# Performance work log

Measured on AMD Instinct MI355X. Metric: run time of the kernel, lower is better.

Reference implementation:

```python
import jax, jax.numpy as jnp
import numpy as np

N = 100000
E = 1600000
F_IN = 128
DIM = 32
NUM_CLASSES = 40
BN_EPS = 1e-5


def setup_inputs() -> dict:
    key = jax.random.key(0)
    ks = jax.random.split(key, 16)
    inp = {}
    inp['x'] = jax.random.normal(ks[0], (N, F_IN), dtype=jnp.float32)
    inp['edge_index'] = jax.random.randint(ks[1], (2, E), 0, N, dtype=jnp.int64)
    s = lambda fan_in: 1.0 / np.sqrt(fan_in)
    # GINConv 1 MLP: Linear(F_IN, DIM) -> ReLU -> Linear(DIM, DIM)
    inp['w1a'] = jax.random.uniform(ks[2], (F_IN, DIM), jnp.float32, -s(F_IN), s(F_IN))
    inp['b1a'] = jnp.zeros((DIM,), jnp.float32)
    inp['w1b'] = jax.random.uniform(ks[3], (DIM, DIM), jnp.float32, -s(DIM), s(DIM))
    inp['b1b'] = jnp.zeros((DIM,), jnp.float32)
    # GINConv 2 MLP: Linear(DIM, DIM) -> ReLU -> Linear(DIM, DIM)
    inp['w2a'] = jax.random.uniform(ks[4], (DIM, DIM), jnp.float32, -s(DIM), s(DIM))
    inp['b2a'] = jnp.zeros((DIM,), jnp.float32)
    inp['w2b'] = jax.random.uniform(ks[5], (DIM, DIM), jnp.float32, -s(DIM), s(DIM))
    inp['b2b'] = jnp.zeros((DIM,), jnp.float32)
    # BatchNorm params (eval mode: running stats)
    inp['bn1_g'] = jnp.ones((DIM,), jnp.float32)
    inp['bn1_b'] = jnp.zeros((DIM,), jnp.float32)
    inp['bn1_m'] = jax.random.normal(ks[6], (DIM,), jnp.float32) * 0.1
    inp['bn1_v'] = jax.random.uniform(ks[7], (DIM,), jnp.float32, 0.5, 1.5)
    inp['bn2_g'] = jnp.ones((DIM,), jnp.float32)
    inp['bn2_b'] = jnp.zeros((DIM,), jnp.float32)
    inp['bn2_m'] = jax.random.normal(ks[8], (DIM,), jnp.float32) * 0.1
    inp['bn2_v'] = jax.random.uniform(ks[9], (DIM,), jnp.float32, 0.5, 1.5)
    # FC heads
    inp['fc1_w'] = jax.random.uniform(ks[10], (DIM, DIM), jnp.float32, -s(DIM), s(DIM))
    inp['fc1_b'] = jnp.zeros((DIM,), jnp.float32)
    inp['fc2_w'] = jax.random.uniform(ks[11], (DIM, NUM_CLASSES), jnp.float32, -s(DIM), s(DIM))
    inp['fc2_b'] = jnp.zeros((NUM_CLASSES,), jnp.float32)
    return inp


def _gin_conv(x, src, dst, wa, ba, wb, bb):
    # sum-aggregate neighbor features (messages flow src -> dst), eps = 0
    agg = jax.ops.segment_sum(x[src], dst, num_segments=N)
    h = agg + x  # (1 + eps) * x + sum_j x_j
    h = jax.nn.relu(h @ wa + ba)
    return h @ wb + bb


def _bn(x, g, b, m, v):
    return (x - m) * (g * jax.lax.rsqrt(v + BN_EPS)) + b


def reference(x, edge_index, w1a, b1a, w1b, b1b, w2a, b2a, w2b, b2b,
              bn1_g, bn1_b, bn1_m, bn1_v, bn2_g, bn2_b, bn2_m, bn2_v,
              fc1_w, fc1_b, fc2_w, fc2_b):
    src, dst = edge_index[0], edge_index[1]
    h = jax.nn.relu(_gin_conv(x, src, dst, w1a, b1a, w1b, b1b))
    h = _bn(h, bn1_g, bn1_b, bn1_m, bn1_v)  # dropout is identity in eval
    h = _gin_conv(h, src, dst, w2a, b2a, w2b, b2b)
    h = _bn(h, bn2_g, bn2_b, bn2_m, bn2_v)
    h = jax.nn.relu(h @ fc1_w + fc1_b)
    logits = h @ fc2_w + fc2_b
    return jax.nn.log_softmax(logits, axis=1)
```

## Files before the change

kernel.cpp:

```cpp
#include <hip/hip_runtime.h>
#include <hip/hip_bf16.h>

static constexpr int N_   = 100000;
static constexpr int E_   = 1600000;
static constexpr int FIN_ = 128;
static constexpr int DIM_ = 32;
static constexpr int NC_  = 40;
static constexpr int NB_BKT = (N_ + 127) / 128;
static constexpr int NCHUNK = 256;
static constexpr int EPC    = E_ / NCHUNK;
static constexpr int NB64P  = 1564;
static constexpr int CS_NB  = (NB_BKT + 7) / 8;

__device__ __forceinline__ int edge_at(const void* e, int is64, long long i) {
    return is64 ? (int)((const long long*)e)[i] : ((const int*)e)[i];
}

__device__ __forceinline__ float bflo(unsigned u) { return __uint_as_float(u << 16); }
__device__ __forceinline__ float bfhi(unsigned u) { return __uint_as_float(u & 0xffff0000u); }

__device__ __forceinline__ unsigned pack2bf(float a, float b) {
    __hip_bfloat16 ha = __float2bfloat16(a), hb = __float2bfloat16(b);
    unsigned ua = *(const unsigned short*)&ha, ub = *(const unsigned short*)&hb;
    return ua | (ub << 16);
}

#define DETECT_FLAG(edge, sflag)                                        \
    if (threadIdx.x < 64) {                                             \
        const long long* p_ = (const long long*)(edge);                 \
        long long v_ = p_[threadIdx.x];                                 \
        bool bad_ = (v_ < 0 || v_ >= (long long)N_);                    \
        unsigned long long m_ = __ballot(bad_);                         \
        if (threadIdx.x == 0) sflag = (m_ == 0ull) ? 1 : 0;             \
    }                                                                   \
    __syncthreads();

__device__ __forceinline__ void stage_acc2(const float* __restrict__ Asm,
                                           const float* __restrict__ Wsm,
                                           int nq, int d0, float4 acc[2]) {
#pragma unroll
    for (int kc = 0; kc < 8; ++kc) {
        float4 w0 = *(const float4*)&Wsm[(kc * 4 + 0) * 32 + d0];
        float4 w1 = *(const float4*)&Wsm[(kc * 4 + 1) * 32 + d0];
        float4 w2 = *(const float4*)&Wsm[(kc * 4 + 2) * 32 + d0];
        float4 w3 = *(const float4*)&Wsm[(kc * 4 + 3) * 32 + d0];
#pragma unroll
        for (int i = 0; i < 2; ++i) {
            float4 a = *(const float4*)&Asm[(nq + 32 * i) * 36 + kc * 4];
            acc[i].x += a.x * w0.x + a.y * w1.x + a.z * w2.x + a.w * w3.x;
            acc[i].y += a.x * w0.y + a.y * w1.y + a.z * w2.y + a.w * w3.y;
            acc[i].z += a.x * w0.z + a.y * w1.z + a.z * w2.z + a.w * w3.z;
            acc[i].w += a.x * w0.w + a.y * w1.w + a.z * w2.w + a.w * w3.w;
        }
    }
}

__global__ __launch_bounds__(256) void chist_kernel(const void* __restrict__ edge,
                                                    int* __restrict__ ghist) {
    __shared__ int lh[NB_BKT];
    __shared__ int sflag;
    DETECT_FLAG(edge, sflag)
    for (int i = threadIdx.x; i < NB_BKT; i += 256) lh[i] = 0;
    __syncthreads();
    int f = sflag;
    int b = blockIdx.x;
    int end = b * EPC + EPC;
    for (int e = b * EPC + threadIdx.x; e < end; e += 256) {
        int d = edge_at(edge, f, (long long)E_ + e);
        atomicAdd(&lh[d >> 7], 1);
    }
    __syncthreads();
    for (int i = threadIdx.x; i < NB_BKT; i += 256) ghist[b * NB_BKT + i] = lh[i];
}

__global__ __launch_bounds__(256) void colscan_kernel(const int* __restrict__ ghist,
                                                      int* __restrict__ gcur,
                                                      int* __restrict__ bcnt,
                                                      int* __restrict__ bbase,
                                                      int* __restrict__ offs,
                                                      int* __restrict__ done) {
    __shared__ int tile[256 * 9];
    __shared__ int a[256];
    __shared__ int lastFlag;
    int tid = threadIdx.x;
    int k0 = blockIdx.x * 8;

    {
        int kk = tid & 7, r0 = tid >> 3;
        for (int p = 0; p < 8; ++p) {
            int b = r0 + p * 32;
            int k = k0 + kk;
            tile[b * 9 + kk] = (k < NB_BKT) ? ghist[b * NB_BKT + k] : 0;
        }
    }
    __syncthreads();

    int c = tid >> 5, lane = tid & 31;
    int v[8]; int s = 0;
#pragma unroll
    for (int r = 0; r < 8; ++r) { v[r] = tile[(lane * 8 + r) * 9 + c]; s += v[r]; }
    int incl = s;
#pragma unroll
    for (int off = 1; off < 32; off <<= 1) {
        int u = __shfl_up(incl, off, 32);
        if (lane >= off) incl += u;
    }
    int ex = incl - s;
    int k = k0 + c;
    if (k < NB_BKT) {
        int run = ex;
#pragma unroll
        for (int r = 0; r < 8; ++r) {
            int b = lane * 8 + r;
            gcur[b * NB_BKT + k] = run;
            run += v[r];
        }
        if (lane == 31) bcnt[k] = run;
    }
    __syncthreads();
    if (tid == 0) {
        __threadfence();
        int old = atomicAdd(done, 1);
        lastFlag = (old == CS_NB - 1) ? 1 : 0;
    }
    __syncthreads();
    if (lastFlag) {
        __threadfence();
        int b4[4]; int base4 = tid * 4; int t = 0;
#pragma unroll
        for (int j = 0; j < 4; ++j) { int i = base4 + j; b4[j] = (i < NB_BKT) ? bcnt[i] : 0; t += b4[j]; }
        a[tid] = t;
        __syncthreads();
        for (int off = 1; off < 256; off <<= 1) {
            int u = a[tid] + ((tid >= off) ? a[tid - off] : 0);
            __syncthreads(); a[tid] = u; __syncthreads();
        }
        int g = a[tid] - t;
#pragma unroll
        for (int j = 0; j < 4; ++j) { int i = base4 + j; if (i < NB_BKT) bbase[i] = g; g += b4[j]; }
        if (tid == 255) offs[N_] = a[255];
    }
}

__global__ __launch_bounds__(256) void dscatter_kernel(const void* __restrict__ edge,
                                                       const int* __restrict__ bbase,
                                                       const int* __restrict__ gcur,
                                                       int* __restrict__ packed) {
    __shared__ int cur[NB_BKT];
    __shared__ int sflag;
    DETECT_FLAG(edge, sflag)
    int b = blockIdx.x, tid = threadIdx.x;
    for (int k = tid; k < NB_BKT; k += 256) cur[k] = bbase[k] + gcur[b * NB_BKT + k];
    __syncthreads();
    int f = sflag;
    int end = b * EPC + EPC;
    for (int e = b * EPC + tid; e < end; e += 256) {
        int s = edge_at(edge, f, e);
        int d = edge_at(edge, f, (long long)E_ + e);
        int pos = atomicAdd(&cur[d >> 7], 1);
        packed[pos] = s | ((d & 127) << 17);
    }
}

__global__ __launch_bounds__(256) void bsort_kernel(const int* __restrict__ bcnt,
                                                    const int* __restrict__ bbase,
                                                    const int* __restrict__ packed,
                                                    int* __restrict__ offs,
                                                    int* __restrict__ csr) {
    __shared__ int c[128];
    __shared__ int cur[128];
    int tid = threadIdx.x;
    int b = blockIdx.x;
    int beg = bbase[b], cnt = bcnt[b];
    if (tid < 128) c[tid] = 0;
    __syncthreads();
    for (int i = tid; i < cnt; i += 256)
        atomicAdd(&c[packed[beg + i] >> 17], 1);
    __syncthreads();
    int myv = (tid < 128) ? c[tid] : 0;
    for (int off = 1; off < 128; off <<= 1) {
        int t = 0;
        if (tid < 128) t = c[tid] + ((tid >= off) ? c[tid - off] : 0);
        __syncthreads();
        if (tid < 128) c[tid] = t;
        __syncthreads();
    }
    if (tid < 128) {
        int ex = c[tid] - myv;
        cur[tid] = ex;
        int node = b * 128 + tid;
        if (node < N_) offs[node] = beg + ex;
    }
    __syncthreads();
    for (int i = tid; i < cnt; i += 256) {
        int v = packed[beg + i];
        int p = atomicAdd(&cur[v >> 17], 1);
        csr[beg + p] = v & 0x1FFFF;
    }
}

__global__ __launch_bounds__(256) void proj_kernel(const float* __restrict__ x,
                                                   const float* __restrict__ w,
                                                   __hip_bfloat16* __restrict__ yh) {
    __shared__ __align__(16) float wsm[FIN_ * DIM_];
    __shared__ __align__(16) float xs[64 * 36];
    int tid = threadIdx.x;
    {
        const float4* w4 = (const float4*)w;
        float4* ws4 = (float4*)wsm;
        for (int i = tid; i < FIN_ * DIM_ / 4; i += 256) ws4[i] = w4[i];
    }
    int nodeBase = blockIdx.x * 64;
    int nq = tid >> 3, dq = tid & 7, d0 = dq * 4;
    const float4* x4 = (const float4*)x;

    float4 acc[2];
    acc[0] = make_float4(0.f, 0.f, 0.f, 0.f);
    acc[1] = make_float4(0.f, 0.f, 0.f, 0.f);

    for (int ch = 0; ch < 4; ++ch) {
        __syncthreads();
#pragma unroll
        for (int p = 0; p < 2; ++p) {
            int idx = tid + 256 * p;
            int row = idx >> 3, c4 = idx & 7;
            int gn = nodeBase + row; if (gn >= N_) gn = N_ - 1;
            *(float4*)&xs[row * 36 + c4 * 4] = x4[(size_t)gn * 32 + ch * 8 + c4];
        }
        __syncthreads();
        stage_acc2(xs, wsm + ch * 32 * DIM_, nq, d0, acc);
    }
#pragma unroll
    for (int i = 0; i < 2; ++i) {
        int gn = nodeBase + nq + 32 * i;
        uint2 pk;
        pk.x = pack2bf(acc[i].x, acc[i].y);
        pk.y = pack2bf(acc[i].z, acc[i].w);
        *(uint2*)((char*)yh + (size_t)gn * 64 + d0 * 2) = pk;
    }
}

__device__ __forceinline__ void gather_row(const int* __restrict__ csr,
                                           const char* __restrict__ vb,
                                           int beg, int end, int loff,
                                           float& a0, float& a1, float& a2, float& a3) {
    int i = beg;
    for (; i + 3 < end; i += 4) {
        int s0 = csr[i], s1 = csr[i + 1], s2 = csr[i + 2], s3 = csr[i + 3];
        uint2 u0 = *(const uint2*)(vb + (((size_t)s0) << 6) + loff);
        uint2 u1 = *(const uint2*)(vb + (((size_t)s1) << 6) + loff);
        uint2 u2 = *(const uint2*)(vb + (((size_t)s2) << 6) + loff);
        uint2 u3 = *(const uint2*)(vb + (((size_t)s3) << 6) + loff);
        a0 += (bflo(u0.x) + bflo(u1.x)) + (bflo(u2.x) + bflo(u3.x));
        a1 += (bfhi(u0.x) + bfhi(u1.x)) + (bfhi(u2.x) + bfhi(u3.x));
        a2 += (bflo(u0.y) + bflo(u1.y)) + (bflo(u2.y) + bflo(u3.y));
        a3 += (bfhi(u0.y) + bfhi(u1.y)) + (bfhi(u2.y) + bfhi(u3.y));
    }
    for (; i < end; ++i) {
        int s0 = csr[i];
        uint2 u0 = *(const uint2*)(vb + (((size_t)s0) << 6) + loff);
        a0 += bflo(u0.x); a1 += bfhi(u0.x); a2 += bflo(u0.y); a3 += bfhi(u0.y);
    }
}

__global__ __launch_bounds__(256) void gathu_kernel(const int* __restrict__ offs,
                                                    const int* __restrict__ csr,
                                                    const __hip_bfloat16* __restrict__ vh,
                                                    const float* __restrict__ bias,
                                                    float* __restrict__ u) {
    int tid = threadIdx.x;
    int nl = tid >> 3, slot = tid & 7;
    int node = blockIdx.x * 32 + nl;
    int beg = offs[node], end = offs[node + 1];
    float a0 = 0.f, a1 = 0.f, a2 = 0.f, a3 = 0.f;
    gather_row(csr, (const char*)vh, beg, end, slot << 3, a0, a1, a2, a3);
    uint2 uy = *(const uint2*)((const char*)vh + (((size_t)node) << 6) + (slot << 3));
    float4 bv = ((const float4*)bias)[slot];
    float4 r;
    r.x = fmaxf(a0 + bflo(uy.x) + bv.x, 0.f);
    r.y = fmaxf(a1 + bfhi(uy.x) + bv.y, 0.f);
    r.z = fmaxf(a2 + bflo(uy.y) + bv.z, 0.f);
    r.w = fmaxf(a3 + bfhi(uy.y) + bv.w, 0.f);
    ((float4*)u)[(size_t)blockIdx.x * 256 + tid] = r;
}

__global__ __launch_bounds__(256) void mlp1_kernel(const float* __restrict__ u,
                                                   const float* __restrict__ w1b,
                                                   const float* __restrict__ b1b,
                                                   const float* __restrict__ g1,
                                                   const float* __restrict__ be1,
                                                   const float* __restrict__ m1,
                                                   const float* __restrict__ v1,
                                                   const float* __restrict__ w2a,
                                                   __hip_bfloat16* __restrict__ zh) {
    __shared__ __align__(16) float A[64 * 36];
    __shared__ float w1s[DIM_ * DIM_];
    __shared__ float w2s[DIM_ * DIM_];
    int tid = threadIdx.x;
    for (int i = tid; i < DIM_ * DIM_; i += 256) { w1s[i] = w1b[i]; w2s[i] = w2a[i]; }
    {
        const float4* u4 = (const float4*)u + (size_t)blockIdx.x * 512;
#pragma unroll
        for (int p = 0; p < 2; ++p) {
            int idx = tid + 256 * p;
            int n = idx >> 3, sl = idx & 7;
            *(float4*)&A[n * 36 + sl * 4] = u4[idx];
        }
    }
    __syncthreads();

    int nq = tid >> 3, dq = tid & 7, d0 = dq * 4;

    float4 gq = *(const float4*)&g1[d0];
    float4 vq = *(const float4*)&v1[d0];
    float4 bq = *(const float4*)&be1[d0];
    float4 mq = *(const float4*)&m1[d0];
    float4 sc, sh;
    sc.x = gq.x * rsqrtf(vq.x + 1e-5f); sc.y = gq.y * rsqrtf(vq.y + 1e-5f);
    sc.z = gq.z * rsqrtf(vq.z + 1e-5f); sc.w = gq.w * rsqrtf(vq.w + 1e-5f);
    sh.x = bq.x - mq.x * sc.x; sh.y = bq.y - mq.y * sc.y;
    sh.z = bq.z - mq.z * sc.z; sh.w = bq.w - mq.w * sc.w;

    float4 h[2];
    {
        float4 bb = *(const float4*)&b1b[d0];
        float4 acc[2] = { bb, bb };
        stage_acc2(A, w1s, nq, d0, acc);
#pragma unroll
        for (int i = 0; i < 2; ++i) {
            h[i].x = fmaxf(acc[i].x, 0.f) * sc.x + sh.x;
            h[i].y = fmaxf(acc[i].y, 0.f) * sc.y + sh.y;
            h[i].z = fmaxf(acc[i].z, 0.f) * sc.z + sh.z;
            h[i].w = fmaxf(acc[i].w, 0.f) * sc.w + sh.w;
        }
    }
    __syncthreads();
#pragma unroll
    for (int i = 0; i < 2; ++i) *(float4*)&A[(nq + 32 * i) * 36 + d0] = h[i];
    __syncthreads();

    {
        float4 acc[2];
        acc[0] = make_float4(0.f, 0.f, 0.f, 0.f);
        acc[1] = make_float4(0.f, 0.f, 0.f, 0.f);
        stage_acc2(A, w2s, nq, d0, acc);
#pragma unroll
        for (int i = 0; i < 2; ++i) {
            int gn = blockIdx.x * 64 + nq + 32 * i;
            uint2 pk;
            pk.x = pack2bf(acc[i].x, acc[i].y);
            pk.y = pack2bf(acc[i].z, acc[i].w);
            *(uint2*)((char*)zh + (size_t)gn * 64 + d0 * 2) = pk;
        }
    }
}

__global__ __launch_bounds__(256) void mlp2_kernel(const float* __restrict__ u,
                                                   const float* __restrict__ w2b,
                                                   const float* __restrict__ b2b,
                                                   const float* __restrict__ g2,
                                                   const float* __restrict__ be2,
                                                   const float* __restrict__ m2,
                                                   const float* __restrict__ v2,
                                                   const float* __restrict__ f1w,
                                                   const float* __restrict__ f1b,
                                                   const float* __restrict__ f2w,
                                                   const float* __restrict__ f2b,
                                                   float* __restrict__ out) {
    __shared__ __align__(16) float A[64 * 36];
    __shared__ float wA[DIM_ * DIM_];
    __shared__ float wB[DIM_ * DIM_];
    __shared__ float wC[DIM_ * NC_];
    int tid = threadIdx.x;
    for (int i = tid; i < DIM_ * DIM_; i += 256) { wA[i] = w2b[i]; wB[i] = f1w[i]; }
    for (int i = tid; i < DIM_ * NC_; i += 256) wC[i] = f2w[i];
    {
        const float4* u4 = (const float4*)u + (size_t)blockIdx.x * 512;
#pragma unroll
        for (int p = 0; p < 2; ++p) {
            int idx = tid + 256 * p;
            int n = idx >> 3, sl = idx & 7;
            *(float4*)&A[n * 36 + sl * 4] = u4[idx];
        }
    }
    __syncthreads();

    int nq = tid >> 3, dq = tid & 7, d0 = dq * 4;

    float4 gq = *(const float4*)&g2[d0];
    float4 vq = *(const float4*)&v2[d0];
    float4 bq = *(const float4*)&be2[d0];
    float4 mq = *(const float4*)&m2[d0];
    float4 sc, sh;
    sc.x = gq.x * rsqrtf(vq.x + 1e-5f); sc.y = gq.y * rsqrtf(vq.y + 1e-5f);
    sc.z = gq.z * rsqrtf(vq.z + 1e-5f); sc.w = gq.w * rsqrtf(vq.w + 1e-5f);
    sh.x = bq.x - mq.x * sc.x; sh.y = bq.y - mq.y * sc.y;
    sh.z = bq.z - mq.z * sc.z; sh.w = bq.w - mq.w * sc.w;

    {
        float4 bb = *(const float4*)&b2b[d0];
        float4 acc[2] = { bb, bb };
        stage_acc2(A, wA, nq, d0, acc);
        float4 h[2];
#pragma unroll
        for (int i = 0; i < 2; ++i) {
            h[i].x = acc[i].x * sc.x + sh.x;
            h[i].y = acc[i].y * sc.y + sh.y;
            h[i].z = acc[i].z * sc.z + sh.z;
            h[i].w = acc[i].w * sc.w + sh.w;
        }
        __syncthreads();
#pragma unroll
        for (int i = 0; i < 2; ++i) *(float4*)&A[(nq + 32 * i) * 36 + d0] = h[i];
        __syncthreads();
    }

    {
        float4 bb = *(const float4*)&f1b[d0];
        float4 acc[2] = { bb, bb };
        stage_acc2(A, wB, nq, d0, acc);
        float4 h[2];
#pragma unroll
        for (int i = 0; i < 2; ++i) {
            h[i].x = fmaxf(acc[i].x, 0.f); h[i].y = fmaxf(acc[i].y, 0.f);
            h[i].z = fmaxf(acc[i].z, 0.f); h[i].w = fmaxf(acc[i].w, 0.f);
        }
        __syncthreads();
#pragma unroll
        for (int i = 0; i < 2; ++i) *(float4*)&A[(nq + 32 * i) * 36 + d0] = h[i];
        __syncthreads();
    }

    {
        float4 bb = *(const float4*)&f2b[d0];
        float be = f2b[32 + dq];
        float4 acc[2] = { bb, bb };
        float acce[2] = { be, be };
#pragma unroll
        for (int kc = 0; kc < 8; ++kc) {
            float4 w0 = *(const float4*)&wC[(kc * 4 + 0) * NC_ + d0];
            float4 w1 = *(const float4*)&wC[(kc * 4 + 1) * NC_ + d0];
            float4 w2 = *(const float4*)&wC[(kc * 4 + 2) * NC_ + d0];
            float4 w3 = *(const float4*)&wC[(kc * 4 + 3) * NC_ + d0];
            float e0 = wC[(kc * 4 + 0) * NC_ + 32 + dq];
            float e1 = wC[(kc * 4 + 1) * NC_ + 32 + dq];
            float e2 = wC[(kc * 4 + 2) * NC_ + 32 + dq];
            float e3 = wC[(kc * 4 + 3) * NC_ + 32 + dq];
#pragma unroll
            for (int i = 0; i < 2; ++i) {
                float4 a = *(const float4*)&A[(nq + 32 * i) * 36 + kc * 4];
                acc[i].x += a.x * w0.x + a.y * w1.x + a.z * w2.x + a.w * w3.x;
                acc[i].y += a.x * w0.y + a.y * w1.y + a.z * w2.y + a.w * w3.y;
                acc[i].z += a.x * w0.z + a.y * w1.z + a.z * w2.z + a.w * w3.z;
                acc[i].w += a.x * w0.w + a.y * w1.w + a.z * w2.w + a.w * w3.w;
                acce[i]  += a.x * e0   + a.y * e1   + a.z * e2   + a.w * e3;
            }
        }
#pragma unroll
        for (int i = 0; i < 2; ++i) {
            float mx = fmaxf(fmaxf(fmaxf(acc[i].x, acc[i].y), fmaxf(acc[i].z, acc[i].w)), acce[i]);
#pragma unroll
            for (int off = 1; off < 8; off <<= 1) mx = fmaxf(mx, __shfl_xor(mx, off, 8));
            float se = __expf(acc[i].x - mx) + __expf(acc[i].y - mx)
                     + __expf(acc[i].z - mx) + __expf(acc[i].w - mx)
                     + __expf(acce[i] - mx);
#pragma unroll
            for (int off = 1; off < 8; off <<= 1) se += __shfl_xor(se, off, 8);
            float lse = mx + __logf(se);
            int gn = blockIdx.x * 64 + nq + 32 * i;
            if (gn < N_) {
                float4 o;
                o.x = acc[i].x - lse; o.y = acc[i].y - lse;
                o.z = acc[i].z - lse; o.w = acc[i].w - lse;
                *(float4*)&out[(size_t)gn * NC_ + d0] = o;
                out[(size_t)gn * NC_ + 32 + dq] = acce[i] - lse;
            }
        }
    }
}

extern "C" void kernel_launch(void* const* d_in, const int* in_sizes, int n_in,
                              void* d_out, int out_size, void* d_ws, size_t ws_size,
                              hipStream_t stream) {
    const float* x   = (const float*)d_in[0];
    const void*  edg = d_in[1];
    const float* w1a = (const float*)d_in[2];
    const float* b1a = (const float*)d_in[3];
    const float* w1b = (const float*)d_in[4];
    const float* b1b = (const float*)d_in[5];
    const float* w2a = (const float*)d_in[6];
    const float* b2a = (const float*)d_in[7];
    const float* w2b = (const float*)d_in[8];
    const float* b2b = (const float*)d_in[9];
    const float* g1  = (const float*)d_in[10];
    const float* be1 = (const float*)d_in[11];
    const float* m1  = (const float*)d_in[12];
    const float* v1  = (const float*)d_in[13];
    const float* g2  = (const float*)d_in[14];
    const float* be2 = (const float*)d_in[15];
    const float* m2  = (const float*)d_in[16];
    const float* v2  = (const float*)d_in[17];
    const float* f1w = (const float*)d_in[18];
    const float* f1b = (const float*)d_in[19];
    const float* f2w = (const float*)d_in[20];
    const float* f2b = (const float*)d_in[21];
    float* out = (float*)d_out;

    char* ws = (char*)d_ws;
    int* done   = (int*)ws;
    int* bcnt   = (int*)(ws + 256);
    int* bbase  = (int*)(ws + 3584);
    int* ghist  = (int*)(ws + 6912);
    int* gcur   = (int*)(ws + 807680);
    int* offs   = (int*)(ws + 1608448);
    int* packed = (int*)(ws + 2008832);
    int* csr    = (int*)(ws + 8408832);
    __hip_bfloat16* yh = (__hip_bfloat16*)(ws + 14808832);
    __hip_bfloat16* zh = (__hip_bfloat16*)(ws + 21214976);
    float* u    = (float*)(ws + 27621120);

    hipMemsetAsync(done, 0, 4, stream);

    chist_kernel<<<NCHUNK, 256, 0, stream>>>(edg, ghist);
    colscan_kernel<<<CS_NB, 256, 0, stream>>>(ghist, gcur, bcnt, bbase, offs, done);
    dscatter_kernel<<<NCHUNK, 256, 0, stream>>>(edg, bbase, gcur, packed);
    bsort_kernel<<<NB_BKT, 256, 0, stream>>>(bcnt, bbase, packed, offs, csr);

    proj_kernel<<<NB64P, 256, 0, stream>>>(x, w1a, yh);

    gathu_kernel<<<N_ / 32, 256, 0, stream>>>(offs, csr, yh, b1a, u);
    mlp1_kernel<<<NB64P, 256, 0, stream>>>(u, w1b, b1b, g1, be1, m1, v1, w2a, zh);

    gathu_kernel<<<N_ / 32, 256, 0, stream>>>(offs, csr, zh, b2a, u);
    mlp2_kernel<<<NB64P, 256, 0, stream>>>(u, w2b, b2b, g2, be2, m2, v2,
                                           f1w, f1b, f2w, f2b, out);
}
```

Measured before the change: 288.1 us.

## Drop per-node CSR sort; aggregate bucketed edges via shared-memory atomics

Removes the bsort kernel that built per-node CSR offsets and sorted sources, and instead aggregates directly from the 128-node bucketed packed edge list. Each block accumulates neighbor bf16 rows into a shared-memory 128x32 tile using float atomics, then adds the self term and bias, applies ReLU and writes out. This saves one kernel launch and the packed-to-csr pass, but adds many LDS atomics per edge in each of the two aggregation passes, and the summation order becomes nondeterministic.

```diff
diff --git a/kernel.cpp b/kernel.cpp
--- a/kernel.cpp
+++ b/kernel.cpp
@@ -77,7 +77,6 @@
                                                       int* __restrict__ gcur,
                                                       int* __restrict__ bcnt,
                                                       int* __restrict__ bbase,
-                                                      int* __restrict__ offs,
                                                       int* __restrict__ done) {
     __shared__ int tile[256 * 9];
     __shared__ int a[256];
@@ -138,7 +137,6 @@
         int g = a[tid] - t;
 #pragma unroll
         for (int j = 0; j < 4; ++j) { int i = base4 + j; if (i < NB_BKT) bbase[i] = g; g += b4[j]; }
-        if (tid == 255) offs[N_] = a[255];
     }
 }
 
@@ -162,43 +160,6 @@
     }
 }
 
-__global__ __launch_bounds__(256) void bsort_kernel(const int* __restrict__ bcnt,
-                                                    const int* __restrict__ bbase,
-                                                    const int* __restrict__ packed,
-                                                    int* __restrict__ offs,
-                                                    int* __restrict__ csr) {
-    __shared__ int c[128];
-    __shared__ int cur[128];
-    int tid = threadIdx.x;
-    int b = blockIdx.x;
-    int beg = bbase[b], cnt = bcnt[b];
-    if (tid < 128) c[tid] = 0;
-    __syncthreads();
-    for (int i = tid; i < cnt; i += 256)
-        atomicAdd(&c[packed[beg + i] >> 17], 1);
-    __syncthreads();
-    int myv = (tid < 128) ? c[tid] : 0;
-    for (int off = 1; off < 128; off <<= 1) {
-        int t = 0;
-        if (tid < 128) t = c[tid] + ((tid >= off) ? c[tid - off] : 0);
-        __syncthreads();
-        if (tid < 128) c[tid] = t;
-        __syncthreads();
-    }
-    if (tid < 128) {
-        int ex = c[tid] - myv;
-        cur[tid] = ex;
-        int node = b * 128 + tid;
-        if (node < N_) offs[node] = beg + ex;
-    }
-    __syncthreads();
-    for (int i = tid; i < cnt; i += 256) {
-        int v = packed[beg + i];
-        int p = atomicAdd(&cur[v >> 17], 1);
-        csr[beg + p] = v & 0x1FFFF;
-    }
-}
-
 __global__ __launch_bounds__(256) void proj_kernel(const float* __restrict__ x,
                                                    const float* __restrict__ w,
                                                    __hip_bfloat16* __restrict__ yh) {
@@ -240,48 +201,62 @@
     }
 }
 
-__device__ __forceinline__ void gather_row(const int* __restrict__ csr,
-                                           const char* __restrict__ vb,
-                                           int beg, int end, int loff,
-                                           float& a0, float& a1, float& a2, float& a3) {
-    int i = beg;
-    for (; i + 3 < end; i += 4) {
-        int s0 = csr[i], s1 = csr[i + 1], s2 = csr[i + 2], s3 = csr[i + 3];
-        uint2 u0 = *(const uint2*)(vb + (((size_t)s0) << 6) + loff);
-        uint2 u1 = *(const uint2*)(vb + (((size_t)s1) << 6) + loff);
-        uint2 u2 = *(const uint2*)(vb + (((size_t)s2) << 6) + loff);
-        uint2 u3 = *(const uint2*)(vb + (((size_t)s3) << 6) + loff);
-        a0 += (bflo(u0.x) + bflo(u1.x)) + (bflo(u2.x) + bflo(u3.x));
-        a1 += (bfhi(u0.x) + bfhi(u1.x)) + (bfhi(u2.x) + bfhi(u3.x));
-        a2 += (bflo(u0.y) + bflo(u1.y)) + (bflo(u2.y) + bflo(u3.y));
-        a3 += (bfhi(u0.y) + bfhi(u1.y)) + (bfhi(u2.y) + bfhi(u3.y));
-    }
-    for (; i < end; ++i) {
-        int s0 = csr[i];
-        uint2 u0 = *(const uint2*)(vb + (((size_t)s0) << 6) + loff);
-        a0 += bflo(u0.x); a1 += bfhi(u0.x); a2 += bflo(u0.y); a3 += bfhi(u0.y);
-    }
-}
-
-__global__ __launch_bounds__(256) void gathu_kernel(const int* __restrict__ offs,
-                                                    const int* __restrict__ csr,
-                                                    const __hip_bfloat16* __restrict__ vh,
-                                                    const float* __restrict__ bias,
-                                                    float* __restrict__ u) {
+__global__ __launch_bounds__(256) void gathagg_kernel(const int* __restrict__ bcnt,
+                                                      const int* __restrict__ bbase,
+                                                      const int* __restrict__ packed,
+                                                      const __hip_bfloat16* __restrict__ vh,
+                                                      const float* __restrict__ bias,
+                                                      float* __restrict__ u) {
+    __shared__ __align__(16) float A[128 * 36];
     int tid = threadIdx.x;
-    int nl = tid >> 3, slot = tid & 7;
-    int node = blockIdx.x * 32 + nl;
-    int beg = offs[node], end = offs[node + 1];
-    float a0 = 0.f, a1 = 0.f, a2 = 0.f, a3 = 0.f;
-    gather_row(csr, (const char*)vh, beg, end, slot << 3, a0, a1, a2, a3);
-    uint2 uy = *(const uint2*)((const char*)vh + (((size_t)node) << 6) + (slot << 3));
-    float4 bv = ((const float4*)bias)[slot];
-    float4 r;
-    r.x = fmaxf(a0 + bflo(uy.x) + bv.x, 0.f);
-    r.y = fmaxf(a1 + bfhi(uy.x) + bv.y, 0.f);
-    r.z = fmaxf(a2 + bflo(uy.y) + bv.z, 0.f);
-    r.w = fmaxf(a3 + bfhi(uy.y) + bv.w, 0.f);
-    ((float4*)u)[(size_t)blockIdx.x * 256 + tid] = r;
+    {
+        float4 z4 = make_float4(0.f, 0.f, 0.f, 0.f);
+        float4* A4 = (float4*)A;
+        for (int i = tid; i < 128 * 9; i += 256) A4[i] = z4;
+    }
+    __syncthreads();
+
+    int b = blockIdx.x;
+    int beg = bbase[b], cnt = bcnt[b];
+    int slot = tid & 3;
+    for (int i = beg + (tid >> 2); i < beg + cnt; i += 64) {
+        int p = packed[i];
+        int src = p & 0x1FFFF;
+        int nl = p >> 17;
+        uint4 v = *(const uint4*)((const char*)vh + (((size_t)src) << 6) + (slot << 4));
+        float* dst = &A[nl * 36 + slot * 8];
+        atomicAdd(dst + 0, bflo(v.x)); atomicAdd(dst + 1, bfhi(v.x));
+        atomicAdd(dst + 2, bflo(v.y)); atomicAdd(dst + 3, bfhi(v.y));
+        atomicAdd(dst + 4, bflo(v.z)); atomicAdd(dst + 5, bfhi(v.z));
+        atomicAdd(dst + 6, bflo(v.w)); atomicAdd(dst + 7, bfhi(v.w));
+    }
+    __syncthreads();
+
+    int nl = tid >> 1, half = tid & 1;
+    int node = b * 128 + nl;
+    if (node >= N_) return;
+    const char* srow = (const char*)vh + (((size_t)node) << 6) + half * 32;
+    uint4 s0 = *(const uint4*)(srow);
+    uint4 s1 = *(const uint4*)(srow + 16);
+    float sf[16];
+    sf[0] = bflo(s0.x); sf[1] = bfhi(s0.x); sf[2]  = bflo(s0.y); sf[3]  = bfhi(s0.y);
+    sf[4] = bflo(s0.z); sf[5] = bfhi(s0.z); sf[6]  = bflo(s0.w); sf[7]  = bfhi(s0.w);
+    sf[8] = bflo(s1.x); sf[9] = bfhi(s1.x); sf[10] = bflo(s1.y); sf[11] = bfhi(s1.y);
+    sf[12]= bflo(s1.z); sf[13]= bfhi(s1.z); sf[14] = bflo(s1.w); sf[15] = bfhi(s1.w);
+    const float4* Ap = (const float4*)&A[nl * 36 + half * 16];
+    const float4* bp = (const float4*)(bias + half * 16);
+    float4* up = (float4*)(u + (size_t)node * 32 + half * 16);
+#pragma unroll
+    for (int q = 0; q < 4; ++q) {
+        float4 av = Ap[q];
+        float4 bv = bp[q];
+        float4 r;
+        r.x = fmaxf(av.x + sf[q * 4 + 0] + bv.x, 0.f);
+        r.y = fmaxf(av.y + sf[q * 4 + 1] + bv.y, 0.f);
+        r.z = fmaxf(av.z + sf[q * 4 + 2] + bv.z, 0.f);
+        r.w = fmaxf(av.w + sf[q * 4 + 3] + bv.w, 0.f);
+        up[q] = r;
+    }
 }
 
 __global__ __launch_bounds__(256) void mlp1_kernel(const float* __restrict__ u,
@@ -512,9 +487,7 @@
     int* bbase  = (int*)(ws + 3584);
     int* ghist  = (int*)(ws + 6912);
     int* gcur   = (int*)(ws + 807680);
-    int* offs   = (int*)(ws + 1608448);
     int* packed = (int*)(ws + 2008832);
-    int* csr    = (int*)(ws + 8408832);
     __hip_bfloat16* yh = (__hip_bfloat16*)(ws + 14808832);
     __hip_bfloat16* zh = (__hip_bfloat16*)(ws + 21214976);
     float* u    = (float*)(ws + 27621120);
@@ -522,16 +495,15 @@
     hipMemsetAsync(done, 0, 4, stream);
 
     chist_kernel<<<NCHUNK, 256, 0, stream>>>(edg, ghist);
-    colscan_kernel<<<CS_NB, 256, 0, stream>>>(ghist, gcur, bcnt, bbase, offs, done);
+    colscan_kernel<<<CS_NB, 256, 0, stream>>>(ghist, gcur, bcnt, bbase, done);
     dscatter_kernel<<<NCHUNK, 256, 0, stream>>>(edg, bbase, gcur, packed);
-    bsort_kernel<<<NB_BKT, 256, 0, stream>>>(bcnt, bbase, packed, offs, csr);
 
     proj_kernel<<<NB64P, 256, 0, stream>>>(x, w1a, yh);
 
-    gathu_kernel<<<N_ / 32, 256, 0, stream>>>(offs, csr, yh, b1a, u);
+    gathagg_kernel<<<NB_BKT, 256, 0, stream>>>(bcnt, bbase, packed, yh, b1a, u);
     mlp1_kernel<<<NB64P, 256, 0, stream>>>(u, w1b, b1b, g1, be1, m1, v1, w2a, zh);
 
-    gathu_kernel<<<N_ / 32, 256, 0, stream>>>(offs, csr, zh, b2a, u);
+    gathagg_kernel<<<NB_BKT, 256, 0, stream>>>(bcnt, bbase, packed, zh, b2a, u);
     mlp2_kernel<<<NB64P, 256, 0, stream>>>(u, w2b, b2b, g2, be2, m2, v2,
                                            f1w, f1b, f2w, f2b, out);
 }
```

Result: slower. 911.0 us (+216.2%).
